# Kernel optimization log

Measured on AMD Instinct MI355X. Metric: run time of the kernel, lower is better.

Reference implementation:

```python
import math
import jax, jax.numpy as jnp
import numpy as np

N, T, D, H, DH = 4, 2048, 1024, 16, 64
CAP = 30.0
EPS = 1e-5


def _layernorm(x, g, b):
    m = jnp.mean(x, axis=-1, keepdims=True)
    v = jnp.mean(jnp.square(x - m), axis=-1, keepdims=True)
    return (x - m) * jax.lax.rsqrt(v + EPS) * g + b


def _rope(x):
    # x: [N, H, t, d]; interleaved rotary (rotary-embedding-torch style), theta=10000
    t, d = x.shape[2], x.shape[3]
    inv_freq = 1.0 / (10000.0 ** (jnp.arange(0, d, 2, dtype=jnp.float32) / d))
    ang = jnp.arange(t, dtype=jnp.float32)[:, None] * inv_freq[None, :]  # [t, d/2]
    cos, sin = jnp.cos(ang), jnp.sin(ang)
    x1, x2 = x[..., 0::2], x[..., 1::2]
    r1 = x1 * cos - x2 * sin
    r2 = x1 * sin + x2 * cos
    return jnp.stack([r1, r2], axis=-1).reshape(x.shape)


def setup_inputs() -> dict:
    key = jax.random.key(0)
    ks = jax.random.split(key, 8)
    s = 0.02
    lengths = jax.random.randint(ks[6], (N,), T // 2, T + 1).astype(jnp.int32)
    key_padding_mask = jnp.arange(T)[None, :] >= lengths[:, None]  # True = pad
    attn_mask = jnp.triu(jnp.ones((T, T), dtype=bool), 1)  # causal: True = masked
    return {
        "x": jax.random.normal(ks[0], (N, T, D), jnp.float32),
        "ln_g": jnp.ones((D,), jnp.float32),
        "ln_b": jnp.zeros((D,), jnp.float32),
        "Wq": jax.random.normal(ks[1], (D, H * DH), jnp.float32) * s,
        "bq": jnp.zeros((H * DH,), jnp.float32),
        "Wk": jax.random.normal(ks[2], (D, H * DH), jnp.float32) * s,
        "bk": jnp.zeros((H * DH,), jnp.float32),
        "Wv": jax.random.normal(ks[3], (D, H * DH), jnp.float32) * s,
        "bv": jnp.zeros((H * DH,), jnp.float32),
        "Wo": jax.random.normal(ks[4], (H * DH, D), jnp.float32) * s,
        "bo": jnp.zeros((D,), jnp.float32),
        "key_padding_mask": key_padding_mask,
        "attn_mask": attn_mask,
        "key_value_sequence_lengths": lengths,
    }


def reference(x, ln_g, ln_b, Wq, bq, Wk, bk, Wv, bv, Wo, bo,
              key_padding_mask, attn_mask, key_value_sequence_lengths):
    n, t, _ = x.shape
    h = _layernorm(x, ln_g, ln_b)  # shared LN for q/k/v (self-attention)
    q = (h @ Wq + bq).reshape(n, t, H, DH).transpose(0, 2, 1, 3)  # [n,H,t,d]
    k = (h @ Wk + bk).reshape(n, t, H, DH).transpose(0, 2, 1, 3)
    v = (h @ Wv + bv).reshape(n, t, H, DH).transpose(0, 2, 1, 3)
    q = _rope(q)
    k = _rope(k)
    scores = jnp.einsum('bhtd,bhTd->bhtT', q, k) / math.sqrt(DH)
    scores = CAP * jnp.tanh(scores / CAP)  # tanh soft-cap
    mask = key_padding_mask[:, None, None, :] | attn_mask[None, None, :, :]
    scores = jnp.where(mask, -jnp.inf, scores)
    attn = jax.nn.softmax(scores, axis=-1)
    out = jnp.einsum('bhtT,bhTd->bhtd', attn, v)
    out = out.transpose(0, 2, 1, 3).reshape(n, t, H * DH)
    return out @ Wo + bo
```

## Files before the change

kernel.cpp:

```cpp
#include <hip/hip_runtime.h>
#include <hip/hip_bf16.h>

typedef unsigned short u16;
typedef unsigned int   u32;
typedef __bf16 bf16x8 __attribute__((ext_vector_type(8)));
typedef float  f32x4  __attribute__((ext_vector_type(4)));

#define NB 4
#define T_ 2048
#define D_ 1024
#define H_ 16
#define DH 64
#define M_ (NB * T_)
#define PSTR 72

__device__ __forceinline__ float bf2f(u16 u) {
    union { u32 i; float f; } v; v.i = ((u32)u) << 16; return v.f;
}
__device__ __forceinline__ u16 f2bf(float f) {
    union { float fl; u32 i; } v; v.fl = f;
    u32 r = v.i + 0x7fff + ((v.i >> 16) & 1);
    return (u16)(r >> 16);
}

__device__ __forceinline__ void gl_lds16(const u16* g, u16* l) {
    __builtin_amdgcn_global_load_lds((const __attribute__((address_space(1))) void*)g,
                                     (__attribute__((address_space(3))) void*)l,
                                     16, 0, 0);
}

__device__ __forceinline__ int detect_f32(const u16* p) {
    int weird = 0;
    const int lane = threadIdx.x & 63;
    #pragma unroll
    for (int i = 0; i < 4; ++i) {
        const u16 u = p[lane * 4 + i];
        const int e = (u >> 7) & 0xFF;
        weird += (e == 0xFF || (e >= 0x01 && e <= 0x3F) || (e >= 0xC0 && e <= 0xFE));
    }
    #pragma unroll
    for (int off = 32; off; off >>= 1) weird += __shfl_xor(weird, off);
    return weird >= 16;
}

__device__ __forceinline__ int read_len(const void* raw, int b) {
    const int* a32 = (const int*)raw;
    bool ok32 = true;
    #pragma unroll
    for (int i = 0; i < NB; ++i) {
        const int v = a32[i];
        if (v < 1 || v > T_) ok32 = false;
    }
    int v = ok32 ? a32[b] : (int)((const long long*)raw)[b];
    return min(max(v, 1), T_);
}

__global__ __launch_bounds__(256) void ln_kernel(const void* __restrict__ xraw,
                                                 const void* __restrict__ graw,
                                                 const void* __restrict__ braw,
                                                 u16* __restrict__ h) {
    const int row = blockIdx.x;
    const int tid = threadIdx.x;
    const int isf = detect_f32((const u16*)xraw);

    float xv[4];
    if (isf) {
        const float* xr = (const float*)xraw + (size_t)row * D_;
        *(float4*)xv = *(const float4*)&xr[tid * 4];
    } else {
        const u16* xr = (const u16*)xraw + (size_t)row * D_;
        u16 loc[4] __attribute__((aligned(8)));
        *(uint2*)loc = *(const uint2*)&xr[tid * 4];
        #pragma unroll
        for (int i = 0; i < 4; ++i) xv[i] = bf2f(loc[i]);
    }

    float s = xv[0] + xv[1] + xv[2] + xv[3];
    float q = xv[0]*xv[0] + xv[1]*xv[1] + xv[2]*xv[2] + xv[3]*xv[3];

    #pragma unroll
    for (int off = 32; off; off >>= 1) {
        s += __shfl_xor(s, off);
        q += __shfl_xor(q, off);
    }
    __shared__ float red[8];
    const int wave = tid >> 6, lane = tid & 63;
    if (lane == 0) { red[wave] = s; red[4 + wave] = q; }
    __syncthreads();
    s = red[0] + red[1] + red[2] + red[3];
    q = red[4] + red[5] + red[6] + red[7];

    const float mean = s * (1.0f / D_);
    const float var  = q * (1.0f / D_) - mean * mean;
    const float rs   = rsqrtf(var + 1e-5f);

    u16 o[4] __attribute__((aligned(8)));
    #pragma unroll
    for (int i = 0; i < 4; ++i) {
        const int c = tid * 4 + i;
        const float gv = isf ? ((const float*)graw)[c] : bf2f(((const u16*)graw)[c]);
        const float bv = isf ? ((const float*)braw)[c] : bf2f(((const u16*)braw)[c]);
        o[i] = f2bf((xv[i] - mean) * rs * gv + bv);
    }
    *(uint2*)&h[(size_t)row * D_ + tid * 4] = *(uint2*)o;
}

__global__ __launch_bounds__(256) void wconv_kernel(const void* __restrict__ Wraw,
                                                    u16* __restrict__ Wt) {
    __shared__ u16 tile[64][PSTR];
    const int isf = detect_f32((const u16*)Wraw);
    const int n0 = blockIdx.x * 64;
    const int k0 = blockIdx.y * 64;
    const int tid = threadIdx.x;
    const int tr  = tid >> 2;
    const int tc  = (tid & 3) * 16;

    if (isf) {
        const float* W = (const float*)Wraw;
        #pragma unroll
        for (int i = 0; i < 16; ++i)
            tile[tc + i][tr] = f2bf(W[(size_t)(k0 + tr) * D_ + n0 + tc + i]);
    } else {
        const u16* W = (const u16*)Wraw;
        #pragma unroll
        for (int i = 0; i < 16; ++i)
            tile[tc + i][tr] = W[(size_t)(k0 + tr) * D_ + n0 + tc + i];
    }
    __syncthreads();
    *(uint4*)&Wt[(size_t)(n0 + tr) * D_ + k0 + tc]     = *(uint4*)&tile[tr][tc];
    *(uint4*)&Wt[(size_t)(n0 + tr) * D_ + k0 + tc + 8] = *(uint4*)&tile[tr][tc + 8];
}

__global__ __launch_bounds__(256) void gemm128_kernel(const u16* __restrict__ A,
                                                      const u16* __restrict__ Bt,
                                                      const void* __restrict__ Braw,
                                                      const void* __restrict__ biasraw,
                                                      void* __restrict__ out,
                                                      const int mode) {
    __shared__ __align__(16) u16 As[128 * 32];
    __shared__ __align__(16) u16 Bs[128 * 32];

    const int tid   = threadIdx.x;
    const int wave  = tid >> 6;
    const int lane  = tid & 63;
    const int quad  = lane >> 4;
    const int lr    = lane & 15;
    const int ntile = blockIdx.x * 128;
    const int mtile = blockIdx.y * 128;

    const int isf = detect_f32((const u16*)Braw);

    const int srow = wave * 32 + (lane >> 2);
    const int scol = (lane & 3) * 8;
    const u16* aptr0 = A  + (size_t)(mtile + srow) * D_ + scol;
    const u16* aptr1 = A  + (size_t)(mtile + srow + 16) * D_ + scol;
    const u16* bptr0 = Bt + (size_t)(ntile + srow) * D_ + scol;
    const u16* bptr1 = Bt + (size_t)(ntile + srow + 16) * D_ + scol;
    u16* alds0 = As + wave * 1024;
    u16* alds1 = As + wave * 1024 + 512;
    u16* blds0 = Bs + wave * 1024;
    u16* blds1 = Bs + wave * 1024 + 512;

    const int mbase = (wave >> 1) * 64;
    const int nbase = (wave & 1) * 64;

    f32x4 acc[4][4];
    #pragma unroll
    for (int m = 0; m < 4; ++m)
        #pragma unroll
        for (int n = 0; n < 4; ++n)
            acc[m][n] = (f32x4){0.f, 0.f, 0.f, 0.f};

    for (int k0 = 0; k0 < D_; k0 += 32) {
        gl_lds16(aptr0 + k0, alds0);
        gl_lds16(aptr1 + k0, alds1);
        gl_lds16(bptr0 + k0, blds0);
        gl_lds16(bptr1 + k0, blds1);
        __syncthreads();

        bf16x8 af[4], bfr[4];
        #pragma unroll
        for (int m = 0; m < 4; ++m)
            af[m] = *(const bf16x8*)&As[(mbase + m * 16 + lr) * 32 + quad * 8];
        #pragma unroll
        for (int n = 0; n < 4; ++n)
            bfr[n] = *(const bf16x8*)&Bs[(nbase + n * 16 + lr) * 32 + quad * 8];
        #pragma unroll
        for (int m = 0; m < 4; ++m)
            #pragma unroll
            for (int n = 0; n < 4; ++n)
                acc[m][n] = __builtin_amdgcn_mfma_f32_16x16x32_bf16(af[m], bfr[n], acc[m][n], 0, 0, 0);

        __syncthreads();
    }

    #pragma unroll
    for (int m = 0; m < 4; ++m) {
        #pragma unroll
        for (int n = 0; n < 4; ++n) {
            const int ncol = ntile + nbase + n * 16 + lr;
            const float bv = isf ? ((const float*)biasraw)[ncol]
                                 : bf2f(((const u16*)biasraw)[ncol]);
            #pragma unroll
            for (int r = 0; r < 4; ++r) {
                const int mrow = mtile + mbase + m * 16 + quad * 4 + r;
                float v = acc[m][n][r] + bv;
                if (mode == 2) {
                    const float other = __shfl_xor(v, 1);
                    const int d = ncol & (DH - 1);
                    const int t = mrow & (T_ - 1);
                    const int i = d >> 1;
                    const float inv = exp2f(-(float)i * 0.41524101186092f);
                    const float ang = (float)t * inv;
                    float sv, cv;
                    __sincosf(ang, &sv, &cv);
                    v = (d & 1) ? (other * sv + v * cv) : (v * cv - other * sv);
                }
                const int d  = ncol & (DH - 1);
                const int hh = ncol >> 6;
                const int t  = mrow & (T_ - 1);
                const int bb = mrow >> 11;
                if (mode == 0) {
                    if (isf) ((float*)out)[(size_t)mrow * D_ + ncol] = v;
                    else     ((u16*)out)[(size_t)mrow * D_ + ncol] = f2bf(v);
                } else if (mode == 1) {
                    ((u16*)out)[(((size_t)(bb * H_ + hh) * DH) + d) * T_ + t] = f2bf(v);
                } else {
                    ((u16*)out)[(((size_t)(bb * H_ + hh) * T_) + t) * DH + d] = f2bf(v);
                }
            }
        }
    }
}

__global__ __launch_bounds__(256) void gemm_kernel(const u16* __restrict__ A,
                                                   const void* __restrict__ Braw,
                                                   const u16* __restrict__ Bt,
                                                   const void* __restrict__ biasraw,
                                                   void* __restrict__ out,
                                                   const int mode) {
    __shared__ __align__(16) u16 As[128 * 32];
    __shared__ __align__(16) u16 Bs[64 * 32];

    const int tid   = threadIdx.x;
    const int ntile = blockIdx.x * 64;
    const int mtile = blockIdx.y * 128;
    const int wave  = tid >> 6;
    const int lane  = tid & 63;
    const int quad  = lane >> 4;
    const int lr    = lane & 15;

    const int isf = detect_f32((const u16*)Braw);
    const float* Bf = (const float*)Braw;
    const u16*   Bu = (const u16*)Braw;

    f32x4 acc[2][4];
    #pragma unroll
    for (int s = 0; s < 2; ++s)
        #pragma unroll
        for (int n = 0; n < 4; ++n)
            acc[s][n] = (f32x4){0.f, 0.f, 0.f, 0.f};

    const int ar  = tid >> 1;
    const int akb = (tid & 1) * 16;
    const int bn  = tid & 63;
    const int bkb = (tid >> 6) * 8;
    const int br  = tid >> 2;
    const int bk2 = (tid & 3) * 8;
    const u16* Arow = A + (size_t)(mtile + ar) * D_ + akb;
    const size_t bcol0 = (size_t)bkb * D_ + ntile + bn;
    const u16* Btrow = Bt ? (Bt + (size_t)(ntile + br) * D_ + bk2) : nullptr;

    for (int k0 = 0; k0 < D_; k0 += 32) {
        *(uint4*)&As[ar * 32 + akb]     = *(const uint4*)(Arow + k0);
        *(uint4*)&As[ar * 32 + akb + 8] = *(const uint4*)(Arow + k0 + 8);
        if (Bt) {
            *(uint4*)&Bs[br * 32 + bk2] = *(const uint4*)(Btrow + k0);
        } else {
            u16 tmp[8] __attribute__((aligned(16)));
            if (isf) {
                #pragma unroll
                for (int j = 0; j < 8; ++j) tmp[j] = f2bf(Bf[bcol0 + (size_t)(k0 + j) * D_]);
            } else {
                #pragma unroll
                for (int j = 0; j < 8; ++j) tmp[j] = Bu[bcol0 + (size_t)(k0 + j) * D_];
            }
            *(uint4*)&Bs[bn * 32 + bkb] = *(uint4*)tmp;
        }
        __syncthreads();

        const int mbase = wave * 32;
        bf16x8 af0 = *(const bf16x8*)&As[(mbase +      lr) * 32 + quad * 8];
        bf16x8 af1 = *(const bf16x8*)&As[(mbase + 16 + lr) * 32 + quad * 8];
        #pragma unroll
        for (int nt = 0; nt < 4; ++nt) {
            bf16x8 bf = *(const bf16x8*)&Bs[(nt * 16 + lr) * 32 + quad * 8];
            acc[0][nt] = __builtin_amdgcn_mfma_f32_16x16x32_bf16(af0, bf, acc[0][nt], 0, 0, 0);
            acc[1][nt] = __builtin_amdgcn_mfma_f32_16x16x32_bf16(af1, bf, acc[1][nt], 0, 0, 0);
        }
        __syncthreads();
    }

    #pragma unroll
    for (int s2 = 0; s2 < 2; ++s2) {
        #pragma unroll
        for (int nt = 0; nt < 4; ++nt) {
            const int ncol = ntile + nt * 16 + lr;
            const float bv = isf ? ((const float*)biasraw)[ncol]
                                 : bf2f(((const u16*)biasraw)[ncol]);
            #pragma unroll
            for (int r = 0; r < 4; ++r) {
                const int mrow = mtile + wave * 32 + s2 * 16 + quad * 4 + r;
                float v = acc[s2][nt][r] + bv;
                if (mode == 2) {
                    const float other = __shfl_xor(v, 1);
                    const int d = ncol & (DH - 1);
                    const int t = mrow & (T_ - 1);
                    const int i = d >> 1;
                    const float inv = exp2f(-(float)i * 0.41524101186092f);
                    const float ang = (float)t * inv;
                    const float cv = cosf(ang), sv = sinf(ang);
                    v = (d & 1) ? (other * sv + v * cv) : (v * cv - other * sv);
                }
                const int d  = ncol & (DH - 1);
                const int hh = ncol >> 6;
                const int t  = mrow & (T_ - 1);
                const int bb = mrow >> 11;
                if (mode == 0) {
                    if (isf) ((float*)out)[(size_t)mrow * D_ + ncol] = v;
                    else     ((u16*)out)[(size_t)mrow * D_ + ncol] = f2bf(v);
                } else if (mode == 1) {
                    ((u16*)out)[(((size_t)(bb * H_ + hh) * DH) + d) * T_ + t] = f2bf(v);
                } else {
                    ((u16*)out)[(((size_t)(bb * H_ + hh) * T_) + t) * DH + d] = f2bf(v);
                }
            }
        }
    }
}

__global__ __launch_bounds__(256) void attn_kernel(const u16* __restrict__ Q,
                                                   const u16* __restrict__ K,
                                                   const u16* __restrict__ Vt,
                                                   const void* __restrict__ lensraw,
                                                   u16* __restrict__ ctx) {
    __shared__ __align__(16) u16 Ps[64 * PSTR];
    __shared__ __align__(16) u16 Ks[64 * PSTR];
    __shared__ __align__(16) u16 Vts[64 * PSTR];

    const int tid  = threadIdx.x;
    const int wave = tid >> 6;
    const int lane = tid & 63;
    const int quad = lane >> 4;
    const int lr   = lane & 15;
    const int bh   = blockIdx.y;
    const int qs   = blockIdx.x * 64;
    const int b    = bh >> 4;
    const int hh   = bh & 15;
    const int len  = read_len(lensraw, b);
    const size_t base = (size_t)bh * T_ * DH;

    const int srow = tid >> 2;
    const int scb  = (tid & 3) * 16;

    *(uint4*)&Ps[srow * PSTR + scb]     = *(const uint4*)&Q[base + (size_t)(qs + srow) * DH + scb];
    *(uint4*)&Ps[srow * PSTR + scb + 8] = *(const uint4*)&Q[base + (size_t)(qs + srow) * DH + scb + 8];
    __syncthreads();
    const bf16x8 qa0 = *(const bf16x8*)&Ps[(wave * 16 + lr) * PSTR + quad * 8];
    const bf16x8 qa1 = *(const bf16x8*)&Ps[(wave * 16 + lr) * PSTR + 32 + quad * 8];

    f32x4 acc[4];
    float l_loc[4] = {0.f, 0.f, 0.f, 0.f};
    #pragma unroll
    for (int nt = 0; nt < 4; ++nt) acc[nt] = (f32x4){0.f, 0.f, 0.f, 0.f};

    const int smax = min(qs + 63, len - 1);
    const int ktn  = smax / 64 + 1;

    for (int kt = 0; kt < ktn; ++kt) {
        const int ks = kt * 64;
        __syncthreads();
        *(uint4*)&Ks[srow * PSTR + scb]      = *(const uint4*)&K[base + (size_t)(ks + srow) * DH + scb];
        *(uint4*)&Ks[srow * PSTR + scb + 8]  = *(const uint4*)&K[base + (size_t)(ks + srow) * DH + scb + 8];
        *(uint4*)&Vts[srow * PSTR + scb]     = *(const uint4*)&Vt[base + (size_t)srow * T_ + ks + scb];
        *(uint4*)&Vts[srow * PSTR + scb + 8] = *(const uint4*)&Vt[base + (size_t)srow * T_ + ks + scb + 8];
        __syncthreads();

        f32x4 s[4];
        #pragma unroll
        for (int nt = 0; nt < 4; ++nt) s[nt] = (f32x4){0.f, 0.f, 0.f, 0.f};
        #pragma unroll
        for (int nt = 0; nt < 4; ++nt) {
            bf16x8 kb0 = *(const bf16x8*)&Ks[(nt * 16 + lr) * PSTR + quad * 8];
            bf16x8 kb1 = *(const bf16x8*)&Ks[(nt * 16 + lr) * PSTR + 32 + quad * 8];
            s[nt] = __builtin_amdgcn_mfma_f32_16x16x32_bf16(qa0, kb0, s[nt], 0, 0, 0);
            s[nt] = __builtin_amdgcn_mfma_f32_16x16x32_bf16(qa1, kb1, s[nt], 0, 0, 0);
        }

        #pragma unroll
        for (int r = 0; r < 4; ++r) {
            const int trow = qs + wave * 16 + quad * 4 + r;
            #pragma unroll
            for (int nt = 0; nt < 4; ++nt) {
                const float z = __expf(s[nt][r] * (1.0f / 120.0f));
                float p = __expf(-60.0f * __builtin_amdgcn_rcpf(z + 1.0f));
                const int col = ks + nt * 16 + lr;
                p = (col > trow || col >= len) ? 0.f : p;
                l_loc[r] += p;
                Ps[(wave * 16 + quad * 4 + r) * PSTR + nt * 16 + lr] = f2bf(p);
            }
        }
        __syncthreads();

        bf16x8 pa0 = *(const bf16x8*)&Ps[(wave * 16 + lr) * PSTR + quad * 8];
        bf16x8 pa1 = *(const bf16x8*)&Ps[(wave * 16 + lr) * PSTR + 32 + quad * 8];
        #pragma unroll
        for (int nt = 0; nt < 4; ++nt) {
            bf16x8 vb0 = *(const bf16x8*)&Vts[(nt * 16 + lr) * PSTR + quad * 8];
            bf16x8 vb1 = *(const bf16x8*)&Vts[(nt * 16 + lr) * PSTR + 32 + quad * 8];
            acc[nt] = __builtin_amdgcn_mfma_f32_16x16x32_bf16(pa0, vb0, acc[nt], 0, 0, 0);
            acc[nt] = __builtin_amdgcn_mfma_f32_16x16x32_bf16(pa1, vb1, acc[nt], 0, 0, 0);
        }
    }

    #pragma unroll
    for (int r = 0; r < 4; ++r) {
        float l = l_loc[r];
        #pragma unroll
        for (int off = 1; off < 16; off <<= 1) l += __shfl_xor(l, off);
        const float invl = (l > 0.f) ? (1.0f / l) : 0.f;
        const int qrow = wave * 16 + quad * 4 + r;
        #pragma unroll
        for (int nt = 0; nt < 4; ++nt) {
            ctx[(size_t)(b * T_ + qs + qrow) * D_ + hh * DH + nt * 16 + lr] =
                f2bf(acc[nt][r] * invl);
        }
    }
}

extern "C" void kernel_launch(void* const* d_in, const int* in_sizes, int n_in,
                              void* d_out, int out_size, void* d_ws, size_t ws_size,
                              hipStream_t stream) {
    u16* h = (u16*)d_ws;
    const size_t MD = (size_t)M_ * D_;
    const size_t WD = (size_t)D_ * D_;
    u16* q  = h + MD;
    u16* k  = q + MD;
    u16* vt = k + MD;
    const bool havewt = ws_size >= (4 * MD + 4 * WD) * sizeof(u16);
    u16* wtq = havewt ? (vt + MD)  : nullptr;
    u16* wtk = havewt ? (wtq + WD) : nullptr;
    u16* wtv = havewt ? (wtk + WD) : nullptr;
    u16* wto = havewt ? (wtv + WD) : nullptr;

    ln_kernel<<<M_, 256, 0, stream>>>(d_in[0], d_in[1], d_in[2], h);

    if (havewt) {
        dim3 wgrid(D_ / 64, D_ / 64);
        wconv_kernel<<<wgrid, 256, 0, stream>>>(d_in[3], wtq);
        wconv_kernel<<<wgrid, 256, 0, stream>>>(d_in[5], wtk);
        wconv_kernel<<<wgrid, 256, 0, stream>>>(d_in[7], wtv);
        wconv_kernel<<<wgrid, 256, 0, stream>>>(d_in[9], wto);

        dim3 g128(D_ / 128, M_ / 128);
        gemm128_kernel<<<g128, 256, 0, stream>>>(h, wtq, d_in[3], d_in[4], q, 2);
        gemm128_kernel<<<g128, 256, 0, stream>>>(h, wtk, d_in[5], d_in[6], k, 2);
        gemm128_kernel<<<g128, 256, 0, stream>>>(h, wtv, d_in[7], d_in[8], vt, 1);

        attn_kernel<<<dim3(T_ / 64, NB * H_), 256, 0, stream>>>(q, k, vt, d_in[13], h);

        gemm128_kernel<<<g128, 256, 0, stream>>>(h, wto, d_in[9], d_in[10], d_out, 0);
    } else {
        dim3 ggrid(D_ / 64, M_ / 128);
        gemm_kernel<<<ggrid, 256, 0, stream>>>(h, d_in[3], nullptr, d_in[4], q, 2);
        gemm_kernel<<<ggrid, 256, 0, stream>>>(h, d_in[5], nullptr, d_in[6], k, 2);
        gemm_kernel<<<ggrid, 256, 0, stream>>>(h, d_in[7], nullptr, d_in[8], vt, 1);

        attn_kernel<<<dim3(T_ / 64, NB * H_), 256, 0, stream>>>(q, k, vt, d_in[13], h);

        gemm_kernel<<<ggrid, 256, 0, stream>>>(h, d_in[9], nullptr, d_in[10], d_out, 0);
    }
}
```

Before: 434.1 us.

## Fuse QKV projections into one GEMM and double-buffer K/V tiles in attention

Replaces the three separate Q/K/V GEMM launches with one qkv_kernel. It covers all three weight matrices through the contiguous transposed-weight buffer, fills LDS with direct global-to-LDS loads, uses 64x64 per-wave MFMA tiles, and applies RoPE and the output layout in the epilogue. The attention kernel now double-buffers K/V tiles in LDS, prefetching the next tile into registers while the current one is computed. It also skips the causal/padding mask arithmetic on tiles that need no masking. This aims to cut launch count, raise MFMA reuse per LDS load, and hide global-load latency, at the cost of more LDS and registers per block.

New measurement: 400.8 us. 1.08x faster.

```diff
diff --git a/kernel.cpp b/kernel.cpp
--- a/kernel.cpp
+++ b/kernel.cpp
@@ -129,6 +129,109 @@
     __syncthreads();
     *(uint4*)&Wt[(size_t)(n0 + tr) * D_ + k0 + tc]     = *(uint4*)&tile[tr][tc];
     *(uint4*)&Wt[(size_t)(n0 + tr) * D_ + k0 + tc + 8] = *(uint4*)&tile[tr][tc + 8];
+}
+
+__global__ __launch_bounds__(256) void qkv_kernel(const u16* __restrict__ A,
+                                                  const u16* __restrict__ Wt3,
+                                                  const void* __restrict__ Braw,
+                                                  const void* __restrict__ bqr,
+                                                  const void* __restrict__ bkr,
+                                                  const void* __restrict__ bvr,
+                                                  u16* __restrict__ qo,
+                                                  u16* __restrict__ ko,
+                                                  u16* __restrict__ vo) {
+    __shared__ __align__(16) u16 As[128 * 32];
+    __shared__ __align__(16) u16 Bs[128 * 32];
+
+    const int tid   = threadIdx.x;
+    const int wave  = tid >> 6;
+    const int lane  = tid & 63;
+    const int quad  = lane >> 4;
+    const int lr    = lane & 15;
+    const int ntile = blockIdx.x * 128;
+    const int mtile = blockIdx.y * 128;
+    const int seg   = ntile >> 10;
+
+    const int isf = detect_f32((const u16*)Braw);
+
+    const int srow = wave * 32 + (lane >> 2);
+    const int scol = (lane & 3) * 8;
+    const u16* aptr0 = A   + (size_t)(mtile + srow) * D_ + scol;
+    const u16* aptr1 = A   + (size_t)(mtile + srow + 16) * D_ + scol;
+    const u16* bptr0 = Wt3 + (size_t)(ntile + srow) * D_ + scol;
+    const u16* bptr1 = Wt3 + (size_t)(ntile + srow + 16) * D_ + scol;
+    u16* alds0 = As + wave * 1024;
+    u16* alds1 = As + wave * 1024 + 512;
+    u16* blds0 = Bs + wave * 1024;
+    u16* blds1 = Bs + wave * 1024 + 512;
+
+    const int mbase = (wave >> 1) * 64;
+    const int nbase = (wave & 1) * 64;
+
+    f32x4 acc[4][4];
+    #pragma unroll
+    for (int m = 0; m < 4; ++m)
+        #pragma unroll
+        for (int n = 0; n < 4; ++n)
+            acc[m][n] = (f32x4){0.f, 0.f, 0.f, 0.f};
+
+    for (int k0 = 0; k0 < D_; k0 += 32) {
+        gl_lds16(aptr0 + k0, alds0);
+        gl_lds16(aptr1 + k0, alds1);
+        gl_lds16(bptr0 + k0, blds0);
+        gl_lds16(bptr1 + k0, blds1);
+        __syncthreads();
+
+        bf16x8 af[4], bfr[4];
+        #pragma unroll
+        for (int m = 0; m < 4; ++m)
+            af[m] = *(const bf16x8*)&As[(mbase + m * 16 + lr) * 32 + quad * 8];
+        #pragma unroll
+        for (int n = 0; n < 4; ++n)
+            bfr[n] = *(const bf16x8*)&Bs[(nbase + n * 16 + lr) * 32 + quad * 8];
+        #pragma unroll
+        for (int m = 0; m < 4; ++m)
+            #pragma unroll
+            for (int n = 0; n < 4; ++n)
+                acc[m][n] = __builtin_amdgcn_mfma_f32_16x16x32_bf16(af[m], bfr[n], acc[m][n], 0, 0, 0);
+
+        __syncthreads();
+    }
+
+    const void* biasraw = (seg == 0) ? bqr : (seg == 1) ? bkr : bvr;
+    u16* out            = (seg == 0) ? qo  : (seg == 1) ? ko  : vo;
+    const int nloc = (ntile & 1023) + nbase;
+
+    #pragma unroll
+    for (int m = 0; m < 4; ++m) {
+        #pragma unroll
+        for (int n = 0; n < 4; ++n) {
+            const int ncl = nloc + n * 16 + lr;
+            const float bv = isf ? ((const float*)biasraw)[ncl]
+                                 : bf2f(((const u16*)biasraw)[ncl]);
+            #pragma unroll
+            for (int r = 0; r < 4; ++r) {
+                const int mrow = mtile + mbase + m * 16 + quad * 4 + r;
+                float v = acc[m][n][r] + bv;
+                const int d  = ncl & (DH - 1);
+                const int hh = ncl >> 6;
+                const int t  = mrow & (T_ - 1);
+                const int bb = mrow >> 11;
+                if (seg < 2) {
+                    const float other = __shfl_xor(v, 1);
+                    const int i = d >> 1;
+                    const float inv = exp2f(-(float)i * 0.41524101186092f);
+                    const float ang = (float)t * inv;
+                    float sv, cv;
+                    __sincosf(ang, &sv, &cv);
+                    v = (d & 1) ? (other * sv + v * cv) : (v * cv - other * sv);
+                    out[(((size_t)(bb * H_ + hh) * T_) + t) * DH + d] = f2bf(v);
+                } else {
+                    out[(((size_t)(bb * H_ + hh) * DH) + d) * T_ + t] = f2bf(v);
+                }
+            }
+        }
+    }
 }
 
 __global__ __launch_bounds__(256) void gemm128_kernel(const u16* __restrict__ A,
@@ -265,18 +368,13 @@
     const int akb = (tid & 1) * 16;
     const int bn  = tid & 63;
     const int bkb = (tid >> 6) * 8;
-    const int br  = tid >> 2;
-    const int bk2 = (tid & 3) * 8;
     const u16* Arow = A + (size_t)(mtile + ar) * D_ + akb;
     const size_t bcol0 = (size_t)bkb * D_ + ntile + bn;
-    const u16* Btrow = Bt ? (Bt + (size_t)(ntile + br) * D_ + bk2) : nullptr;
 
     for (int k0 = 0; k0 < D_; k0 += 32) {
         *(uint4*)&As[ar * 32 + akb]     = *(const uint4*)(Arow + k0);
         *(uint4*)&As[ar * 32 + akb + 8] = *(const uint4*)(Arow + k0 + 8);
-        if (Bt) {
-            *(uint4*)&Bs[br * 32 + bk2] = *(const uint4*)(Btrow + k0);
-        } else {
+        {
             u16 tmp[8] __attribute__((aligned(16)));
             if (isf) {
                 #pragma unroll
@@ -345,8 +443,8 @@
                                                    const void* __restrict__ lensraw,
                                                    u16* __restrict__ ctx) {
     __shared__ __align__(16) u16 Ps[64 * PSTR];
-    __shared__ __align__(16) u16 Ks[64 * PSTR];
-    __shared__ __align__(16) u16 Vts[64 * PSTR];
+    __shared__ __align__(16) u16 Ks[2][64 * PSTR];
+    __shared__ __align__(16) u16 Vts[2][64 * PSTR];
 
     const int tid  = threadIdx.x;
     const int wave = tid >> 6;
@@ -362,12 +460,25 @@
 
     const int srow = tid >> 2;
     const int scb  = (tid & 3) * 16;
+    const u16* Kb = K + base;
+    const u16* Vb = Vt + base;
 
     *(uint4*)&Ps[srow * PSTR + scb]     = *(const uint4*)&Q[base + (size_t)(qs + srow) * DH + scb];
     *(uint4*)&Ps[srow * PSTR + scb + 8] = *(const uint4*)&Q[base + (size_t)(qs + srow) * DH + scb + 8];
+    {
+        uint4 k0 = *(const uint4*)&Kb[(size_t)srow * DH + scb];
+        uint4 k1 = *(const uint4*)&Kb[(size_t)srow * DH + scb + 8];
+        uint4 v0 = *(const uint4*)&Vb[(size_t)srow * T_ + scb];
+        uint4 v1 = *(const uint4*)&Vb[(size_t)srow * T_ + scb + 8];
+        *(uint4*)&Ks[0][srow * PSTR + scb]      = k0;
+        *(uint4*)&Ks[0][srow * PSTR + scb + 8]  = k1;
+        *(uint4*)&Vts[0][srow * PSTR + scb]     = v0;
+        *(uint4*)&Vts[0][srow * PSTR + scb + 8] = v1;
+    }
     __syncthreads();
     const bf16x8 qa0 = *(const bf16x8*)&Ps[(wave * 16 + lr) * PSTR + quad * 8];
     const bf16x8 qa1 = *(const bf16x8*)&Ps[(wave * 16 + lr) * PSTR + 32 + quad * 8];
+    __syncthreads();
 
     f32x4 acc[4];
     float l_loc[4] = {0.f, 0.f, 0.f, 0.f};
@@ -376,38 +487,58 @@
 
     const int smax = min(qs + 63, len - 1);
     const int ktn  = smax / 64 + 1;
-
+    const int prow = wave * 16 + quad * 4;
+
+    int buf = 0;
+    uint4 kr0, kr1, vr0, vr1;
     for (int kt = 0; kt < ktn; ++kt) {
         const int ks = kt * 64;
-        __syncthreads();
-        *(uint4*)&Ks[srow * PSTR + scb]      = *(const uint4*)&K[base + (size_t)(ks + srow) * DH + scb];
-        *(uint4*)&Ks[srow * PSTR + scb + 8]  = *(const uint4*)&K[base + (size_t)(ks + srow) * DH + scb + 8];
-        *(uint4*)&Vts[srow * PSTR + scb]     = *(const uint4*)&Vt[base + (size_t)srow * T_ + ks + scb];
-        *(uint4*)&Vts[srow * PSTR + scb + 8] = *(const uint4*)&Vt[base + (size_t)srow * T_ + ks + scb + 8];
-        __syncthreads();
+        const bool havenext = (kt + 1 < ktn);
+
+        if (havenext) {
+            const int ns = ks + 64;
+            kr0 = *(const uint4*)&Kb[(size_t)(ns + srow) * DH + scb];
+            kr1 = *(const uint4*)&Kb[(size_t)(ns + srow) * DH + scb + 8];
+            vr0 = *(const uint4*)&Vb[(size_t)srow * T_ + ns + scb];
+            vr1 = *(const uint4*)&Vb[(size_t)srow * T_ + ns + scb + 8];
+        }
 
         f32x4 s[4];
         #pragma unroll
         for (int nt = 0; nt < 4; ++nt) s[nt] = (f32x4){0.f, 0.f, 0.f, 0.f};
         #pragma unroll
         for (int nt = 0; nt < 4; ++nt) {
-            bf16x8 kb0 = *(const bf16x8*)&Ks[(nt * 16 + lr) * PSTR + quad * 8];
-            bf16x8 kb1 = *(const bf16x8*)&Ks[(nt * 16 + lr) * PSTR + 32 + quad * 8];
+            bf16x8 kb0 = *(const bf16x8*)&Ks[buf][(nt * 16 + lr) * PSTR + quad * 8];
+            bf16x8 kb1 = *(const bf16x8*)&Ks[buf][(nt * 16 + lr) * PSTR + 32 + quad * 8];
             s[nt] = __builtin_amdgcn_mfma_f32_16x16x32_bf16(qa0, kb0, s[nt], 0, 0, 0);
             s[nt] = __builtin_amdgcn_mfma_f32_16x16x32_bf16(qa1, kb1, s[nt], 0, 0, 0);
         }
 
-        #pragma unroll
-        for (int r = 0; r < 4; ++r) {
-            const int trow = qs + wave * 16 + quad * 4 + r;
+        const bool need_mask = (ks == qs) || (ks + 63 >= len);
+        if (!need_mask) {
             #pragma unroll
-            for (int nt = 0; nt < 4; ++nt) {
-                const float z = __expf(s[nt][r] * (1.0f / 120.0f));
-                float p = __expf(-60.0f * __builtin_amdgcn_rcpf(z + 1.0f));
-                const int col = ks + nt * 16 + lr;
-                p = (col > trow || col >= len) ? 0.f : p;
-                l_loc[r] += p;
-                Ps[(wave * 16 + quad * 4 + r) * PSTR + nt * 16 + lr] = f2bf(p);
+            for (int r = 0; r < 4; ++r) {
+                #pragma unroll
+                for (int nt = 0; nt < 4; ++nt) {
+                    const float z = __expf(s[nt][r] * (1.0f / 120.0f));
+                    const float p = __expf(-60.0f * __builtin_amdgcn_rcpf(z + 1.0f));
+                    l_loc[r] += p;
+                    Ps[(prow + r) * PSTR + nt * 16 + lr] = f2bf(p);
+                }
+            }
+        } else {
+            #pragma unroll
+            for (int r = 0; r < 4; ++r) {
+                const int trow = qs + prow + r;
+                #pragma unroll
+                for (int nt = 0; nt < 4; ++nt) {
+                    const float z = __expf(s[nt][r] * (1.0f / 120.0f));
+                    float p = __expf(-60.0f * __builtin_amdgcn_rcpf(z + 1.0f));
+                    const int col = ks + nt * 16 + lr;
+                    p = (col > trow || col >= len) ? 0.f : p;
+                    l_loc[r] += p;
+                    Ps[(prow + r) * PSTR + nt * 16 + lr] = f2bf(p);
+                }
             }
         }
         __syncthreads();
@@ -416,11 +547,20 @@
         bf16x8 pa1 = *(const bf16x8*)&Ps[(wave * 16 + lr) * PSTR + 32 + quad * 8];
         #pragma unroll
         for (int nt = 0; nt < 4; ++nt) {
-            bf16x8 vb0 = *(const bf16x8*)&Vts[(nt * 16 + lr) * PSTR + quad * 8];
-            bf16x8 vb1 = *(const bf16x8*)&Vts[(nt * 16 + lr) * PSTR + 32 + quad * 8];
+            bf16x8 vb0 = *(const bf16x8*)&Vts[buf][(nt * 16 + lr) * PSTR + quad * 8];
+            bf16x8 vb1 = *(const bf16x8*)&Vts[buf][(nt * 16 + lr) * PSTR + 32 + quad * 8];
             acc[nt] = __builtin_amdgcn_mfma_f32_16x16x32_bf16(pa0, vb0, acc[nt], 0, 0, 0);
             acc[nt] = __builtin_amdgcn_mfma_f32_16x16x32_bf16(pa1, vb1, acc[nt], 0, 0, 0);
         }
+
+        if (havenext) {
+            *(uint4*)&Ks[buf ^ 1][srow * PSTR + scb]      = kr0;
+            *(uint4*)&Ks[buf ^ 1][srow * PSTR + scb + 8]  = kr1;
+            *(uint4*)&Vts[buf ^ 1][srow * PSTR + scb]     = vr0;
+            *(uint4*)&Vts[buf ^ 1][srow * PSTR + scb + 8] = vr1;
+        }
+        __syncthreads();
+        buf ^= 1;
     }
 
     #pragma unroll
@@ -429,7 +569,7 @@
         #pragma unroll
         for (int off = 1; off < 16; off <<= 1) l += __shfl_xor(l, off);
         const float invl = (l > 0.f) ? (1.0f / l) : 0.f;
-        const int qrow = wave * 16 + quad * 4 + r;
+        const int qrow = prow + r;
         #pragma unroll
         for (int nt = 0; nt < 4; ++nt) {
             ctx[(size_t)(b * T_ + qs + qrow) * D_ + hh * DH + nt * 16 + lr] =
@@ -462,14 +602,13 @@
         wconv_kernel<<<wgrid, 256, 0, stream>>>(d_in[7], wtv);
         wconv_kernel<<<wgrid, 256, 0, stream>>>(d_in[9], wto);
 
-        dim3 g128(D_ / 128, M_ / 128);
-        gemm128_kernel<<<g128, 256, 0, stream>>>(h, wtq, d_in[3], d_in[4], q, 2);
-        gemm128_kernel<<<g128, 256, 0, stream>>>(h, wtk, d_in[5], d_in[6], k, 2);
-        gemm128_kernel<<<g128, 256, 0, stream>>>(h, wtv, d_in[7], d_in[8], vt, 1);
+        qkv_kernel<<<dim3(3 * D_ / 128, M_ / 128), 256, 0, stream>>>(
+            h, wtq, d_in[3], d_in[4], d_in[6], d_in[8], q, k, vt);
 
         attn_kernel<<<dim3(T_ / 64, NB * H_), 256, 0, stream>>>(q, k, vt, d_in[13], h);
 
-        gemm128_kernel<<<g128, 256, 0, stream>>>(h, wto, d_in[9], d_in[10], d_out, 0);
+        gemm128_kernel<<<dim3(D_ / 128, M_ / 128), 256, 0, stream>>>(
+            h, wto, d_in[9], d_in[10], d_out, 0);
     } else {
         dim3 ggrid(D_ / 64, M_ / 128);
         gemm_kernel<<<ggrid, 256, 0, stream>>>(h, d_in[3], nullptr, d_in[4], q, 2);
```
